# Kernel optimization log

Measured on AMD Instinct MI355X. Metric: run time of the kernel, lower is better.

The kernel has to match this reference:

```python
import jax, jax.numpy as jnp
import numpy as np

N, E, B, D, DEPTH = 20000, 160000, 16, 128, 5
L = 4 * DEPTH  # 20 EGNN layer calls: (ground, ground_to_sub, sub, sub_to_ground) x depth


def _ln(x, g, b):
    mu = jnp.mean(x, -1, keepdims=True)
    var = jnp.mean((x - mu) ** 2, -1, keepdims=True)
    return (x - mu) * jax.lax.rsqrt(var + 1e-5) * g + b


def setup_inputs() -> dict:
    key = jax.random.key(0)
    ks = jax.random.split(key, 24)

    def w(k, shape, fan_in):
        return jax.random.normal(k, shape, jnp.float32) / np.float32(np.sqrt(fan_in))

    return {
        "x": jax.random.normal(ks[0], (N, 1), jnp.float32),
        "pos": jax.random.normal(ks[1], (N, 3), jnp.float32),
        "edge_index": jax.random.randint(ks[2], (2, E), 0, N),
        "node_subnode_index": jax.random.randint(ks[3], (2, E), 0, N),
        "subgraph_edge_index": jax.random.randint(ks[4], (2, E), 0, N),
        "subnode_node_index": jax.random.randint(ks[5], (2, E), 0, N),
        "batch_ids": jnp.sort(jax.random.randint(ks[6], (N,), 0, B)),
        "emb_W": w(ks[7], (1, D), 1), "emb_b": jnp.zeros((D,), jnp.float32),
        # message MLP: Linear(2D+1,D) -> LN -> SiLU -> Linear(D,D) -> LN -> SiLU, stacked over L layers
        "Wm1": w(ks[8], (L, 2 * D + 1, D), 2 * D + 1), "bm1": jnp.zeros((L, D), jnp.float32),
        "gm1": jnp.ones((L, D), jnp.float32), "sm1": jnp.zeros((L, D), jnp.float32),
        "Wm2": w(ks[9], (L, D, D), D), "bm2": jnp.zeros((L, D), jnp.float32),
        "gm2": jnp.ones((L, D), jnp.float32), "sm2": jnp.zeros((L, D), jnp.float32),
        # update MLP: Linear(2D,D) -> LN -> SiLU -> Linear(D,D) -> LN -> SiLU
        "Wu1": w(ks[10], (L, 2 * D, D), 2 * D), "bu1": jnp.zeros((L, D), jnp.float32),
        "gu1": jnp.ones((L, D), jnp.float32), "su1": jnp.zeros((L, D), jnp.float32),
        "Wu2": w(ks[11], (L, D, D), D), "bu2": jnp.zeros((L, D), jnp.float32),
        "gu2": jnp.ones((L, D), jnp.float32), "su2": jnp.zeros((L, D), jnp.float32),
        # prediction head: Linear(D,D) -> ReLU -> Linear(D,1)
        "pred_W1": w(ks[12], (D, D), D), "pred_b1": jnp.zeros((D,), jnp.float32),
        "pred_W2": w(ks[13], (D, 1), D), "pred_b2": jnp.zeros((1,), jnp.float32),
    }


def _egnn(h, pos, ei, i, Wm1, bm1, gm1, sm1, Wm2, bm2, gm2, sm2,
          Wu1, bu1, gu1, su1, Wu2, bu2, gu2, su2):
    src, dst = ei[0], ei[1]          # PyG: messages flow source -> target
    rel = pos[dst] - pos[src]
    dist = jnp.sqrt(jnp.sum(rel * rel, -1, keepdims=True))  # [E,1]
    m = jnp.concatenate([h[dst], h[src], dist], -1)          # [E, 2D+1] = [h_i, h_j, d]
    m = jax.nn.silu(_ln(m @ Wm1[i] + bm1[i], gm1[i], sm1[i]))
    m = jax.nn.silu(_ln(m @ Wm2[i] + bm2[i], gm2[i], sm2[i]))
    agg = jax.ops.segment_sum(m, dst, num_segments=h.shape[0])
    u = jnp.concatenate([h, agg], -1)                        # [N, 2D]
    u = jax.nn.silu(_ln(u @ Wu1[i] + bu1[i], gu1[i], su1[i]))
    u = jax.nn.silu(_ln(u @ Wu2[i] + bu2[i], gu2[i], su2[i]))
    return u


def reference(x, pos, edge_index, node_subnode_index, subgraph_edge_index,
              subnode_node_index, batch_ids, emb_W, emb_b,
              Wm1, bm1, gm1, sm1, Wm2, bm2, gm2, sm2,
              Wu1, bu1, gu1, su1, Wu2, bu2, gu2, su2,
              pred_W1, pred_b1, pred_W2, pred_b2):
    p = (Wm1, bm1, gm1, sm1, Wm2, bm2, gm2, sm2,
         Wu1, bu1, gu1, su1, Wu2, bu2, gu2, su2)
    h = x @ emb_W + emb_b
    edge_sets = (edge_index, node_subnode_index, subgraph_edge_index, subnode_node_index)
    for layer_idx in range(DEPTH):
        h0 = h
        for r, ei in enumerate(edge_sets):
            h = _egnn(h, pos, ei, layer_idx * 4 + r, *p)
        h = h + h0  # residual across the 4 message-passing steps
    out = jax.ops.segment_sum(h, batch_ids, num_segments=B)  # global_add_pool
    return jax.nn.relu(out @ pred_W1 + pred_b1) @ pred_W2 + pred_b2
```

## Files before the change

### kernel.cpp

```cpp
#include <hip/hip_runtime.h>

#define NN 20000
#define NE 160000
#define NL 20

typedef float f32x4 __attribute__((ext_vector_type(4)));
typedef float f32x2 __attribute__((ext_vector_type(2)));
typedef __bf16 bf16x8 __attribute__((ext_vector_type(8)));
typedef __bf16 bf16x4 __attribute__((ext_vector_type(4)));

__device__ __forceinline__ float silu_f(float v) {
  return v * __builtin_amdgcn_rcpf(1.f + __expf(-v));
}

__global__ void pack_weights(const float* __restrict__ W, __bf16* __restrict__ out,
                             const int K, const int lstride, const int total) {
  const int idx = blockIdx.x * 256 + threadIdx.x;
  if (idx >= total) return;
  const int lane = idx & 63;
  const int nt = (idx >> 6) & 7;
  const int ktn = K >> 5;
  const int kt = (idx >> 9) % ktn;
  const int layer = (idx >> 9) / ktn;
  const int col = nt * 16 + (lane & 15);
  const int kb = kt * 32 + (lane >> 4) * 8;
  const float* src = W + (size_t)layer * lstride;
  __bf16* o = out + (size_t)idx * 8;
#pragma unroll
  for (int j = 0; j < 8; ++j) o[j] = (__bf16)src[(kb + j) * 128 + col];
}

__global__ void pack_w1pq(const float* __restrict__ Wm1, __bf16* __restrict__ out) {
  const int idx = blockIdx.x * 256 + threadIdx.x;
  const int lane = idx & 63;
  const int nt = (idx >> 6) & 15;
  const int kt = (idx >> 10) & 3;
  const int layer = idx >> 12;
  const int c = nt * 16 + (lane & 15);
  const int kb = kt * 32 + (lane >> 4) * 8;
  const float* src = Wm1 + (size_t)layer * 257 * 128;
  __bf16* o = out + (size_t)idx * 8;
#pragma unroll
  for (int j = 0; j < 8; ++j) {
    const int k = kb + j;
    o[j] = (__bf16)((c < 128) ? src[k * 128 + c] : src[(128 + k) * 128 + (c - 128)]);
  }
}

__global__ void embed_kernel(const float* __restrict__ x, const float* __restrict__ embW,
                             const float* __restrict__ embB,
                             float* __restrict__ h, float* __restrict__ h0,
                             __bf16* __restrict__ hbf) {
  const int idx = blockIdx.x * 256 + threadIdx.x;
  const int n = idx >> 7, d = idx & 127;
  const float v = x[n] * embW[d] + embB[d];
  h[idx] = v;
  h0[idx] = v;
  hbf[idx] = (__bf16)v;
}

__global__ void hist_kernel(const int* __restrict__ ei, int* __restrict__ deg) {
  const int e = blockIdx.x * 256 + threadIdx.x;
  atomicAdd(&deg[ei[NE + e]], 1);
}

__global__ void scan_kernel(const int* __restrict__ deg, int* __restrict__ rowstart) {
  __shared__ int part[1024];
  const int r = blockIdx.x, t = threadIdx.x;
  const int* d = deg + (size_t)r * NN;
  int* rs = rowstart + (size_t)r * NN;
  int loc[20];
  int cnt = 0;
#pragma unroll
  for (int j = 0; j < 20; ++j) {
    const int i = t * 20 + j;
    const int v = (i < NN) ? d[i] : 0;
    loc[j] = cnt; cnt += v;
  }
  part[t] = cnt;
  __syncthreads();
  for (int off = 1; off < 1024; off <<= 1) {
    const int v = (t >= off) ? part[t - off] : 0;
    __syncthreads();
    part[t] += v;
    __syncthreads();
  }
  const int excl = (t == 0) ? 0 : part[t - 1];
#pragma unroll
  for (int j = 0; j < 20; ++j) {
    const int i = t * 20 + j;
    if (i < NN) rs[i] = excl + loc[j];
  }
}

__global__ void fill_kernel(const int* __restrict__ ei, const int* __restrict__ rowstart,
                            int* __restrict__ cursor, int* __restrict__ eord) {
  const int e = blockIdx.x * 256 + threadIdx.x;
  const int d = ei[NE + e];
  const int p = atomicAdd(&cursor[d], 1);
  eord[rowstart[d] + p] = e;
}

__global__ __launch_bounds__(256) void pq_kernel(
    const __bf16* __restrict__ hbf, const __bf16* __restrict__ pqw,
    __bf16* __restrict__ pq) {
  __shared__ __bf16 T1s[4][2048];
  const int t = threadIdx.x, w = t >> 6, l = t & 63;
  const int lr = l & 15, lg = l >> 4;
  const int wid = blockIdx.x * 4 + w;
  const int n0 = (wid >> 1) * 16;
  const int half = wid & 1;
  char* T1 = (char*)T1s[w];

  const int node = n0 + lr;
  bf16x8 bq[4];
#pragma unroll
  for (int kt = 0; kt < 4; ++kt)
    bq[kt] = *(const bf16x8*)(hbf + (size_t)node * 128 + kt * 32 + lg * 8);

  f32x4 acc[8];
#pragma unroll
  for (int nt = 0; nt < 8; ++nt) acc[nt] = (f32x4)0.f;
#pragma unroll
  for (int kt = 0; kt < 4; ++kt) {
#pragma unroll
    for (int nt = 0; nt < 8; ++nt) {
      const bf16x8 a = *(const bf16x8*)(pqw + ((size_t)((kt * 16 + half * 8 + nt) * 64 + l)) * 8);
      acc[nt] = __builtin_amdgcn_mfma_f32_16x16x32_bf16(a, bq[kt], acc[nt], 0, 0, 0);
    }
  }
#pragma unroll
  for (int nt = 0; nt < 8; ++nt) {
    bf16x4 v;
#pragma unroll
    for (int r = 0; r < 4; ++r) v[r] = (__bf16)acc[nt][r];
    *(bf16x4*)(T1 + ((lr * 256 + nt * 32 + lg * 8) ^ ((lr & 7) << 4))) = v;
  }
  __builtin_amdgcn_s_waitcnt(0);
#pragma unroll
  for (int j = 0; j < 4; ++j) {
    const int row = j * 4 + lg;
    const uint4 v = *(const uint4*)(T1 + ((row * 256 + lr * 16) ^ ((row & 7) << 4)));
    *(uint4*)(pq + (size_t)(n0 + row) * 256 + half * 128 + lr * 8) = v;
  }
}

__global__ __launch_bounds__(1024, 4) void edge_msg_kernel(
    const __bf16* __restrict__ pq, const float* __restrict__ pos,
    const int* __restrict__ ei, __bf16* __restrict__ msg,
    const __bf16* __restrict__ w2p, const float* __restrict__ w1last,
    const float* __restrict__ bm1, const float* __restrict__ gm1, const float* __restrict__ sm1,
    const float* __restrict__ bm2, const float* __restrict__ gm2, const float* __restrict__ sm2) {
  extern __shared__ char lds[];
  {
    const int t = threadIdx.x;
    uint4* d = (uint4*)lds;
    const uint4* s2 = (const uint4*)w2p;
    d[t] = s2[t];
    d[t + 1024] = s2[t + 1024];
  }
  __syncthreads();

  const int t = threadIdx.x, w = t >> 6, l = t & 63;
  const int lr = l & 15, lg = l >> 4;
  char* W2L = lds;
  char* T1  = lds + 32768 + w * 4096;

  const int e0 = blockIdx.x * 256 + w * 16;
  const int es = ei[e0 + lr], ed = ei[NE + e0 + lr];
  const float dx = pos[ed * 3 + 0] - pos[es * 3 + 0];
  const float dy = pos[ed * 3 + 1] - pos[es * 3 + 1];
  const float dz = pos[ed * 3 + 2] - pos[es * 3 + 2];
  const float dist = sqrtf(dx * dx + dy * dy + dz * dz);

  float v[4][8];
#pragma unroll
  for (int kt = 0; kt < 4; ++kt) {
    const int d0 = kt * 32 + lg * 8;
    const bf16x8 pA = *(const bf16x8*)(pq + (size_t)ed * 256 + d0);
    const bf16x8 qA = *(const bf16x8*)(pq + (size_t)es * 256 + 128 + d0);
    const f32x4 wl0 = *(const f32x4*)(w1last + d0), wl1 = *(const f32x4*)(w1last + d0 + 4);
    const f32x4 bb0 = *(const f32x4*)(bm1 + d0),    bb1 = *(const f32x4*)(bm1 + d0 + 4);
#pragma unroll
    for (int j = 0; j < 4; ++j) {
      v[kt][j]     = (float)pA[j]     + (float)qA[j]     + dist * wl0[j] + bb0[j];
      v[kt][j + 4] = (float)pA[j + 4] + (float)qA[j + 4] + dist * wl1[j] + bb1[j];
    }
  }
  float s = 0.f, q = 0.f;
#pragma unroll
  for (int kt = 0; kt < 4; ++kt)
#pragma unroll
    for (int j = 0; j < 8; ++j) { const float x = v[kt][j]; s += x; q += x * x; }
  s += __shfl_xor(s, 16); q += __shfl_xor(q, 16);
  s += __shfl_xor(s, 32); q += __shfl_xor(q, 32);
  const float mu1 = s * 0.0078125f;
  const float rstd1 = rsqrtf(q * 0.0078125f - mu1 * mu1 + 1e-5f);
  bf16x8 bfrag[4];
#pragma unroll
  for (int kt = 0; kt < 4; ++kt) {
    const int d0 = kt * 32 + lg * 8;
    const f32x4 g0 = *(const f32x4*)(gm1 + d0), g1 = *(const f32x4*)(gm1 + d0 + 4);
    const f32x4 s0 = *(const f32x4*)(sm1 + d0), s1 = *(const f32x4*)(sm1 + d0 + 4);
    bf16x8 bf;
#pragma unroll
    for (int j = 0; j < 4; ++j) {
      bf[j]     = (__bf16)silu_f((v[kt][j]     - mu1) * rstd1 * g0[j] + s0[j]);
      bf[j + 4] = (__bf16)silu_f((v[kt][j + 4] - mu1) * rstd1 * g1[j] + s1[j]);
    }
    bfrag[kt] = bf;
  }
  f32x4 acc2[8];
#pragma unroll
  for (int nt = 0; nt < 8; ++nt)
    acc2[nt] = *(const f32x4*)(bm2 + nt * 16 + lg * 4);
#pragma unroll
  for (int kt = 0; kt < 4; ++kt) {
#pragma unroll
    for (int nt = 0; nt < 8; ++nt) {
      const bf16x8 a = *(const bf16x8*)(W2L + ((kt * 8 + nt) * 64 + l) * 16);
      acc2[nt] = __builtin_amdgcn_mfma_f32_16x16x32_bf16(a, bfrag[kt], acc2[nt], 0, 0, 0);
    }
  }
  float s2 = 0.f, q2 = 0.f;
#pragma unroll
  for (int nt = 0; nt < 8; ++nt)
#pragma unroll
    for (int r = 0; r < 4; ++r) { const float x = acc2[nt][r]; s2 += x; q2 += x * x; }
  s2 += __shfl_xor(s2, 16); q2 += __shfl_xor(q2, 16);
  s2 += __shfl_xor(s2, 32); q2 += __shfl_xor(q2, 32);
  const float mu2 = s2 * 0.0078125f;
  const float rstd2 = rsqrtf(q2 * 0.0078125f - mu2 * mu2 + 1e-5f);
#pragma unroll
  for (int nt = 0; nt < 8; ++nt) {
    const f32x4 g2 = *(const f32x4*)(gm2 + nt * 16 + lg * 4);
    const f32x4 b2 = *(const f32x4*)(sm2 + nt * 16 + lg * 4);
    bf16x4 pk;
#pragma unroll
    for (int r = 0; r < 4; ++r)
      pk[r] = (__bf16)silu_f((acc2[nt][r] - mu2) * rstd2 * g2[r] + b2[r]);
    *(bf16x4*)(T1 + ((lr * 256 + nt * 32 + lg * 8) ^ ((lr & 7) << 4))) = pk;
  }
  __builtin_amdgcn_s_waitcnt(0);
  char* mbase = (char*)(msg + (size_t)e0 * 128);
#pragma unroll
  for (int j = 0; j < 4; ++j) {
    const int row = j * 4 + lg;
    const uint4 val = *(const uint4*)(T1 + ((row * 256 + lr * 16) ^ ((row & 7) << 4)));
    *(uint4*)(mbase + j * 1024 + l * 16) = val;
  }
}

__global__ void gather_kernel(const __bf16* __restrict__ msg,
                              const int* __restrict__ rowstart, const int* __restrict__ deg,
                              const int* __restrict__ eord, float* __restrict__ agg) {
  const int t = blockIdx.x * 256 + threadIdx.x;
  const int n = t >> 6, pd = t & 63;
  const int s = rowstart[n], dg = deg[n];
  float a0 = 0.f, a1 = 0.f;
  int i = 0;
  for (; i + 2 <= dg; i += 2) {
    const unsigned v0 = *(const unsigned*)(msg + (size_t)eord[s + i] * 128 + pd * 2);
    const unsigned v1 = *(const unsigned*)(msg + (size_t)eord[s + i + 1] * 128 + pd * 2);
    a0 += __uint_as_float(v0 << 16) + __uint_as_float(v1 << 16);
    a1 += __uint_as_float(v0 & 0xFFFF0000u) + __uint_as_float(v1 & 0xFFFF0000u);
  }
  if (i < dg) {
    const unsigned v0 = *(const unsigned*)(msg + (size_t)eord[s + i] * 128 + pd * 2);
    a0 += __uint_as_float(v0 << 16);
    a1 += __uint_as_float(v0 & 0xFFFF0000u);
  }
  f32x2 o; o[0] = a0; o[1] = a1;
  *(f32x2*)(agg + (size_t)n * 128 + pd * 2) = o;
}

__global__ __launch_bounds__(256) void update_kernel(
    float* __restrict__ h, const float* __restrict__ aggv, __bf16* __restrict__ hbf,
    float* __restrict__ h0, const int mode,
    const __bf16* __restrict__ w1p, const __bf16* __restrict__ w2p,
    const float* __restrict__ bu1, const float* __restrict__ gu1, const float* __restrict__ su1,
    const float* __restrict__ bu2, const float* __restrict__ gu2, const float* __restrict__ su2) {
  __shared__ __bf16 T1s[4][16 * 128];
  const int t = threadIdx.x, w = t >> 6, l = t & 63;
  const int lr = l & 15, lg = l >> 4;
  char* T1 = (char*)T1s[w];
  const int n0 = blockIdx.x * 64 + w * 16;
  const int n = n0 + lr;
  const int valid = (n < NN);
  const int nc = valid ? n : 0;

  bf16x8 ah[4], af[4];
#pragma unroll
  for (int kt = 0; kt < 4; ++kt) {
    ah[kt] = *(const bf16x8*)(hbf + (size_t)nc * 128 + kt * 32 + lg * 8);
    const f32x4* pA = (const f32x4*)(aggv + (size_t)nc * 128 + kt * 32 + lg * 8);
    const f32x4 u0 = pA[0], u1 = pA[1];
#pragma unroll
    for (int j = 0; j < 4; ++j) {
      af[kt][j] = (__bf16)u0[j];
      af[kt][j + 4] = (__bf16)u1[j];
    }
  }
  f32x4 acc[8];
#pragma unroll
  for (int nt = 0; nt < 8; ++nt) {
    const float bb = bu1[nt * 16 + lr];
#pragma unroll
    for (int r = 0; r < 4; ++r) acc[nt][r] = bb;
  }
#pragma unroll
  for (int kt = 0; kt < 8; ++kt) {
    const bf16x8 a = (kt < 4) ? ah[kt] : af[kt - 4];
#pragma unroll
    for (int nt = 0; nt < 8; ++nt) {
      const bf16x8 b = *(const bf16x8*)(w1p + ((size_t)((kt * 8 + nt) * 64 + l)) * 8);
      acc[nt] = __builtin_amdgcn_mfma_f32_16x16x32_bf16(a, b, acc[nt], 0, 0, 0);
    }
  }
  {
    float g1c[8], s1c[8];
#pragma unroll
    for (int nt = 0; nt < 8; ++nt) { g1c[nt] = gu1[nt * 16 + lr]; s1c[nt] = su1[nt * 16 + lr]; }
#pragma unroll
    for (int r = 0; r < 4; ++r) {
      float s = 0.f, q = 0.f;
#pragma unroll
      for (int nt = 0; nt < 8; ++nt) { const float v = acc[nt][r]; s += v; q += v * v; }
#pragma unroll
      for (int m = 1; m < 16; m <<= 1) { s += __shfl_xor(s, m); q += __shfl_xor(q, m); }
      const float mu = s * 0.0078125f;
      const float rstd = rsqrtf(q * 0.0078125f - mu * mu + 1e-5f);
      const int row = lg * 4 + r;
#pragma unroll
      for (int nt = 0; nt < 8; ++nt) {
        float v = (acc[nt][r] - mu) * rstd * g1c[nt] + s1c[nt];
        v = silu_f(v);
        const int col = nt * 16 + lr;
        *(__bf16*)(T1 + ((row * 256 + col * 2) ^ ((row & 7) << 4))) = (__bf16)v;
      }
    }
  }
  __syncthreads();
  f32x4 acc2[8];
#pragma unroll
  for (int nt = 0; nt < 8; ++nt) {
    const float bb = bu2[nt * 16 + lr];
#pragma unroll
    for (int r = 0; r < 4; ++r) acc2[nt][r] = bb;
  }
#pragma unroll
  for (int kt = 0; kt < 4; ++kt) {
    const bf16x8 a = *(const bf16x8*)(T1 + ((lr * 256 + kt * 64 + lg * 16) ^ ((lr & 7) << 4)));
#pragma unroll
    for (int nt = 0; nt < 8; ++nt) {
      const bf16x8 b = *(const bf16x8*)(w2p + ((size_t)((kt * 8 + nt) * 64 + l)) * 8);
      acc2[nt] = __builtin_amdgcn_mfma_f32_16x16x32_bf16(a, b, acc2[nt], 0, 0, 0);
    }
  }
  {
    float g2c[8], s2c[8];
#pragma unroll
    for (int nt = 0; nt < 8; ++nt) { g2c[nt] = gu2[nt * 16 + lr]; s2c[nt] = su2[nt * 16 + lr]; }
#pragma unroll
    for (int r = 0; r < 4; ++r) {
      float s = 0.f, q = 0.f;
#pragma unroll
      for (int nt = 0; nt < 8; ++nt) { const float v = acc2[nt][r]; s += v; q += v * v; }
#pragma unroll
      for (int m = 1; m < 16; m <<= 1) { s += __shfl_xor(s, m); q += __shfl_xor(q, m); }
      const float mu = s * 0.0078125f;
      const float rstd = rsqrtf(q * 0.0078125f - mu * mu + 1e-5f);
      const int row = lg * 4 + r;
      const int nn = n0 + row;
      if (nn < NN) {
#pragma unroll
        for (int nt = 0; nt < 8; ++nt) {
          const int col = nt * 16 + lr;
          float v = (acc2[nt][r] - mu) * rstd * g2c[nt] + s2c[nt];
          v = silu_f(v);
          if (mode) v += h0[(size_t)nn * 128 + col];
          h[(size_t)nn * 128 + col] = v;
          hbf[(size_t)nn * 128 + col] = (__bf16)v;
          if (mode) h0[(size_t)nn * 128 + col] = v;
        }
      }
    }
  }
}

__global__ void pool_kernel(const float* __restrict__ h, const int* __restrict__ bid,
                            float* __restrict__ pooled) {
  const int d = threadIdx.x;
  const int n0 = blockIdx.x * 32;
  const int nend = (n0 + 32 < NN) ? (n0 + 32) : NN;
  float acc = 0.f;
  int cur = bid[n0];
  for (int n = n0; n < nend; ++n) {
    const int b = bid[n];
    if (b != cur) { atomicAdd(&pooled[cur * 128 + d], acc); acc = 0.f; cur = b; }
    acc += h[(size_t)n * 128 + d];
  }
  atomicAdd(&pooled[cur * 128 + d], acc);
}

__global__ void head_kernel(const float* __restrict__ pooled,
                            const float* __restrict__ W1, const float* __restrict__ b1,
                            const float* __restrict__ W2, const float* __restrict__ b2,
                            float* __restrict__ out) {
  __shared__ float buf[2];
  const int b = blockIdx.x, t = threadIdx.x;
  float s = b1[t];
  for (int k = 0; k < 128; ++k) s += pooled[b * 128 + k] * W1[k * 128 + t];
  s = fmaxf(s, 0.f) * W2[t];
#pragma unroll
  for (int m = 32; m >= 1; m >>= 1) s += __shfl_down(s, m);
  if ((t & 63) == 0) buf[t >> 6] = s;
  __syncthreads();
  if (t == 0) out[b] = buf[0] + buf[1] + b2[0];
}

extern "C" void kernel_launch(void* const* d_in, const int* in_sizes, int n_in,
                              void* d_out, int out_size, void* d_ws, size_t ws_size,
                              hipStream_t stream) {
  const float* x   = (const float*)d_in[0];
  const float* pos = (const float*)d_in[1];
  const int* eis[4] = {(const int*)d_in[2], (const int*)d_in[3],
                       (const int*)d_in[4], (const int*)d_in[5]};
  const int* bid = (const int*)d_in[6];
  const float* embW = (const float*)d_in[7];
  const float* embB = (const float*)d_in[8];
  const float* Wm1 = (const float*)d_in[9];
  const float* bm1 = (const float*)d_in[10];
  const float* gm1 = (const float*)d_in[11];
  const float* sm1 = (const float*)d_in[12];
  const float* Wm2 = (const float*)d_in[13];
  const float* bm2 = (const float*)d_in[14];
  const float* gm2 = (const float*)d_in[15];
  const float* sm2 = (const float*)d_in[16];
  const float* Wu1 = (const float*)d_in[17];
  const float* bu1 = (const float*)d_in[18];
  const float* gu1 = (const float*)d_in[19];
  const float* su1 = (const float*)d_in[20];
  const float* Wu2 = (const float*)d_in[21];
  const float* bu2 = (const float*)d_in[22];
  const float* gu2 = (const float*)d_in[23];
  const float* su2 = (const float*)d_in[24];
  const float* pW1 = (const float*)d_in[25];
  const float* pb1 = (const float*)d_in[26];
  const float* pW2 = (const float*)d_in[27];
  const float* pb2 = (const float*)d_in[28];
  float* out = (float*)d_out;

  char* wp = (char*)d_ws;
  float* h = (float*)wp;      wp += (size_t)NN * 128 * 4;
  float* h0 = (float*)wp;     wp += (size_t)NN * 128 * 4;
  float* agg = (float*)wp;    wp += (size_t)NN * 128 * 4;
  float* pooled = (float*)wp; wp += 16 * 128 * 4;
  __bf16* hbf = (__bf16*)wp;  wp += (size_t)NN * 128 * 2;
  __bf16* pq = (__bf16*)wp;   wp += (size_t)NN * 256 * 2;
  __bf16* msg = (__bf16*)wp;  wp += (size_t)NE * 128 * 2;
  __bf16* pqw = (__bf16*)wp;  wp += (size_t)NL * 32768 * 2;
  __bf16* w2p = (__bf16*)wp;  wp += (size_t)NL * 16384 * 2;
  __bf16* wu1p = (__bf16*)wp; wp += (size_t)NL * 32768 * 2;
  __bf16* wu2p = (__bf16*)wp; wp += (size_t)NL * 16384 * 2;
  int* deg = (int*)wp;        wp += (size_t)4 * NN * 4;
  int* cursor = (int*)wp;     wp += (size_t)4 * NN * 4;
  int* rowstart = (int*)wp;   wp += (size_t)4 * NN * 4;
  int* eord = (int*)wp;       wp += (size_t)4 * NE * 4;

  static int lds_attr_set = 0;
  if (!lds_attr_set) {
    hipFuncSetAttribute((const void*)edge_msg_kernel,
                        hipFuncAttributeMaxDynamicSharedMemorySize, 98304);
    lds_attr_set = 1;
  }

  pack_w1pq<<<320, 256, 0, stream>>>(Wm1, pqw);
  pack_weights<<<160, 256, 0, stream>>>(Wm2, w2p, 128, 128 * 128, NL * 4 * 8 * 64);
  pack_weights<<<320, 256, 0, stream>>>(Wu1, wu1p, 256, 256 * 128, NL * 8 * 8 * 64);
  pack_weights<<<160, 256, 0, stream>>>(Wu2, wu2p, 128, 128 * 128, NL * 4 * 8 * 64);

  hipMemsetAsync(deg, 0, (size_t)8 * NN * 4, stream);
  embed_kernel<<<(NN * 128) / 256, 256, 0, stream>>>(x, embW, embB, h, h0, hbf);
  for (int r = 0; r < 4; ++r)
    hist_kernel<<<NE / 256, 256, 0, stream>>>(eis[r], deg + (size_t)r * NN);
  scan_kernel<<<4, 1024, 0, stream>>>(deg, rowstart);
  for (int r = 0; r < 4; ++r)
    fill_kernel<<<NE / 256, 256, 0, stream>>>(eis[r], rowstart + (size_t)r * NN,
                                              cursor + (size_t)r * NN, eord + (size_t)r * NE);

  for (int layer = 0; layer < 5; ++layer) {
    for (int r = 0; r < 4; ++r) {
      const int i = layer * 4 + r;
      pq_kernel<<<625, 256, 0, stream>>>(hbf, pqw + (size_t)i * 32768, pq);
      edge_msg_kernel<<<NE / 256, 1024, 98304, stream>>>(
          pq, pos, eis[r], msg,
          w2p + (size_t)i * 16384,
          Wm1 + (size_t)i * 257 * 128 + 256 * 128,
          bm1 + i * 128, gm1 + i * 128, sm1 + i * 128,
          bm2 + i * 128, gm2 + i * 128, sm2 + i * 128);
      gather_kernel<<<(NN * 64) / 256, 256, 0, stream>>>(
          msg, rowstart + (size_t)r * NN, deg + (size_t)r * NN, eord + (size_t)r * NE, agg);
      update_kernel<<<(NN + 63) / 64, 256, 0, stream>>>(
          h, agg, hbf, h0, (r == 3) ? 1 : 0,
          wu1p + (size_t)i * 32768, wu2p + (size_t)i * 16384,
          bu1 + i * 128, gu1 + i * 128, su1 + i * 128,
          bu2 + i * 128, gu2 + i * 128, su2 + i * 128);
    }
  }

  hipMemsetAsync(pooled, 0, 16 * 128 * 4, stream);
  pool_kernel<<<(NN + 31) / 32, 128, 0, stream>>>(h, bid, pooled);
  head_kernel<<<16, 128, 0, stream>>>(pooled, pW1, pb1, pW2, pb2, out);
}
```

Measured before the change: 1.944 ms.

## Make edge message kernel persistent with register prefetch of next tile

```diff
diff --git a/kernel.cpp b/kernel.cpp
--- a/kernel.cpp
+++ b/kernel.cpp
@@ -136,7 +136,6 @@
     for (int r = 0; r < 4; ++r) v[r] = (__bf16)acc[nt][r];
     *(bf16x4*)(T1 + ((lr * 256 + nt * 32 + lg * 8) ^ ((lr & 7) << 4))) = v;
   }
-  __builtin_amdgcn_s_waitcnt(0);
 #pragma unroll
   for (int j = 0; j < 4; ++j) {
     const int row = j * 4 + lg;
@@ -166,88 +165,120 @@
   char* W2L = lds;
   char* T1  = lds + 32768 + w * 4096;
 
-  const int e0 = blockIdx.x * 256 + w * 16;
-  const int es = ei[e0 + lr], ed = ei[NE + e0 + lr];
-  const float dx = pos[ed * 3 + 0] - pos[es * 3 + 0];
-  const float dy = pos[ed * 3 + 1] - pos[es * 3 + 1];
-  const float dz = pos[ed * 3 + 2] - pos[es * 3 + 2];
-  const float dist = sqrtf(dx * dx + dy * dy + dz * dz);
-
-  float v[4][8];
+  const int NW = gridDim.x * 16;
+  const int NT = NE / 16;
+  int tile = blockIdx.x * 16 + w;
+
+  int es = ei[tile * 16 + lr], ed = ei[NE + tile * 16 + lr];
+  float dist;
+  {
+    const float dx = pos[ed * 3 + 0] - pos[es * 3 + 0];
+    const float dy = pos[ed * 3 + 1] - pos[es * 3 + 1];
+    const float dz = pos[ed * 3 + 2] - pos[es * 3 + 2];
+    dist = sqrtf(dx * dx + dy * dy + dz * dz);
+  }
+  bf16x8 pA[4], qA[4];
 #pragma unroll
   for (int kt = 0; kt < 4; ++kt) {
-    const int d0 = kt * 32 + lg * 8;
-    const bf16x8 pA = *(const bf16x8*)(pq + (size_t)ed * 256 + d0);
-    const bf16x8 qA = *(const bf16x8*)(pq + (size_t)es * 256 + 128 + d0);
-    const f32x4 wl0 = *(const f32x4*)(w1last + d0), wl1 = *(const f32x4*)(w1last + d0 + 4);
-    const f32x4 bb0 = *(const f32x4*)(bm1 + d0),    bb1 = *(const f32x4*)(bm1 + d0 + 4);
+    pA[kt] = *(const bf16x8*)(pq + (size_t)ed * 256 + kt * 32 + lg * 8);
+    qA[kt] = *(const bf16x8*)(pq + (size_t)es * 256 + 128 + kt * 32 + lg * 8);
+  }
+
+  while (true) {
+    const int next = tile + NW;
+    const bool more = (next < NT);
+    float dist_n = 0.f;
+    bf16x8 pA_n[4], qA_n[4];
+    if (more) {
+      const int es_n = ei[next * 16 + lr], ed_n = ei[NE + next * 16 + lr];
+      const float dx = pos[ed_n * 3 + 0] - pos[es_n * 3 + 0];
+      const float dy = pos[ed_n * 3 + 1] - pos[es_n * 3 + 1];
+      const float dz = pos[ed_n * 3 + 2] - pos[es_n * 3 + 2];
+      dist_n = sqrtf(dx * dx + dy * dy + dz * dz);
+#pragma unroll
+      for (int kt = 0; kt < 4; ++kt) {
+        pA_n[kt] = *(const bf16x8*)(pq + (size_t)ed_n * 256 + kt * 32 + lg * 8);
+        qA_n[kt] = *(const bf16x8*)(pq + (size_t)es_n * 256 + 128 + kt * 32 + lg * 8);
+      }
+    }
+    float v[4][8];
+#pragma unroll
+    for (int kt = 0; kt < 4; ++kt) {
+      const int d0 = kt * 32 + lg * 8;
+      const f32x4 wl0 = *(const f32x4*)(w1last + d0), wl1 = *(const f32x4*)(w1last + d0 + 4);
+      const f32x4 bb0 = *(const f32x4*)(bm1 + d0),    bb1 = *(const f32x4*)(bm1 + d0 + 4);
+#pragma unroll
+      for (int j = 0; j < 4; ++j) {
+        v[kt][j]     = (float)pA[kt][j]     + (float)qA[kt][j]     + dist * wl0[j] + bb0[j];
+        v[kt][j + 4] = (float)pA[kt][j + 4] + (float)qA[kt][j + 4] + dist * wl1[j] + bb1[j];
+      }
+    }
+    float s = 0.f, q = 0.f;
+#pragma unroll
+    for (int kt = 0; kt < 4; ++kt)
+#pragma unroll
+      for (int j = 0; j < 8; ++j) { const float x = v[kt][j]; s += x; q += x * x; }
+    s += __shfl_xor(s, 16); q += __shfl_xor(q, 16);
+    s += __shfl_xor(s, 32); q += __shfl_xor(q, 32);
+    const float mu1 = s * 0.0078125f;
+    const float rstd1 = rsqrtf(q * 0.0078125f - mu1 * mu1 + 1e-5f);
+    bf16x8 bfrag[4];
+#pragma unroll
+    for (int kt = 0; kt < 4; ++kt) {
+      const int d0 = kt * 32 + lg * 8;
+      const f32x4 g0 = *(const f32x4*)(gm1 + d0), g1 = *(const f32x4*)(gm1 + d0 + 4);
+      const f32x4 s0 = *(const f32x4*)(sm1 + d0), s1 = *(const f32x4*)(sm1 + d0 + 4);
+      bf16x8 bf;
+#pragma unroll
+      for (int j = 0; j < 4; ++j) {
+        bf[j]     = (__bf16)silu_f((v[kt][j]     - mu1) * rstd1 * g0[j] + s0[j]);
+        bf[j + 4] = (__bf16)silu_f((v[kt][j + 4] - mu1) * rstd1 * g1[j] + s1[j]);
+      }
+      bfrag[kt] = bf;
+    }
+    f32x4 acc2[8];
+#pragma unroll
+    for (int nt = 0; nt < 8; ++nt)
+      acc2[nt] = *(const f32x4*)(bm2 + nt * 16 + lg * 4);
+#pragma unroll
+    for (int kt = 0; kt < 4; ++kt) {
+#pragma unroll
+      for (int nt = 0; nt < 8; ++nt) {
+        const bf16x8 a = *(const bf16x8*)(W2L + ((kt * 8 + nt) * 64 + l) * 16);
+        acc2[nt] = __builtin_amdgcn_mfma_f32_16x16x32_bf16(a, bfrag[kt], acc2[nt], 0, 0, 0);
+      }
+    }
+    float s2 = 0.f, q2 = 0.f;
+#pragma unroll
+    for (int nt = 0; nt < 8; ++nt)
+#pragma unroll
+      for (int r = 0; r < 4; ++r) { const float x = acc2[nt][r]; s2 += x; q2 += x * x; }
+    s2 += __shfl_xor(s2, 16); q2 += __shfl_xor(q2, 16);
+    s2 += __shfl_xor(s2, 32); q2 += __shfl_xor(q2, 32);
+    const float mu2 = s2 * 0.0078125f;
+    const float rstd2 = rsqrtf(q2 * 0.0078125f - mu2 * mu2 + 1e-5f);
+#pragma unroll
+    for (int nt = 0; nt < 8; ++nt) {
+      const f32x4 g2 = *(const f32x4*)(gm2 + nt * 16 + lg * 4);
+      const f32x4 b2 = *(const f32x4*)(sm2 + nt * 16 + lg * 4);
+      bf16x4 pk;
+#pragma unroll
+      for (int r = 0; r < 4; ++r)
+        pk[r] = (__bf16)silu_f((acc2[nt][r] - mu2) * rstd2 * g2[r] + b2[r]);
+      *(bf16x4*)(T1 + ((lr * 256 + nt * 32 + lg * 8) ^ ((lr & 7) << 4))) = pk;
+    }
+    char* mbase = (char*)(msg + (size_t)(tile * 16) * 128);
 #pragma unroll
     for (int j = 0; j < 4; ++j) {
-      v[kt][j]     = (float)pA[j]     + (float)qA[j]     + dist * wl0[j] + bb0[j];
-      v[kt][j + 4] = (float)pA[j + 4] + (float)qA[j + 4] + dist * wl1[j] + bb1[j];
-    }
-  }
-  float s = 0.f, q = 0.f;
-#pragma unroll
-  for (int kt = 0; kt < 4; ++kt)
-#pragma unroll
-    for (int j = 0; j < 8; ++j) { const float x = v[kt][j]; s += x; q += x * x; }
-  s += __shfl_xor(s, 16); q += __shfl_xor(q, 16);
-  s += __shfl_xor(s, 32); q += __shfl_xor(q, 32);
-  const float mu1 = s * 0.0078125f;
-  const float rstd1 = rsqrtf(q * 0.0078125f - mu1 * mu1 + 1e-5f);
-  bf16x8 bfrag[4];
-#pragma unroll
-  for (int kt = 0; kt < 4; ++kt) {
-    const int d0 = kt * 32 + lg * 8;
-    const f32x4 g0 = *(const f32x4*)(gm1 + d0), g1 = *(const f32x4*)(gm1 + d0 + 4);
-    const f32x4 s0 = *(const f32x4*)(sm1 + d0), s1 = *(const f32x4*)(sm1 + d0 + 4);
-    bf16x8 bf;
-#pragma unroll
-    for (int j = 0; j < 4; ++j) {
-      bf[j]     = (__bf16)silu_f((v[kt][j]     - mu1) * rstd1 * g0[j] + s0[j]);
-      bf[j + 4] = (__bf16)silu_f((v[kt][j + 4] - mu1) * rstd1 * g1[j] + s1[j]);
-    }
-    bfrag[kt] = bf;
-  }
-  f32x4 acc2[8];
-#pragma unroll
-  for (int nt = 0; nt < 8; ++nt)
-    acc2[nt] = *(const f32x4*)(bm2 + nt * 16 + lg * 4);
-#pragma unroll
-  for (int kt = 0; kt < 4; ++kt) {
-#pragma unroll
-    for (int nt = 0; nt < 8; ++nt) {
-      const bf16x8 a = *(const bf16x8*)(W2L + ((kt * 8 + nt) * 64 + l) * 16);
-      acc2[nt] = __builtin_amdgcn_mfma_f32_16x16x32_bf16(a, bfrag[kt], acc2[nt], 0, 0, 0);
-    }
-  }
-  float s2 = 0.f, q2 = 0.f;
-#pragma unroll
-  for (int nt = 0; nt < 8; ++nt)
-#pragma unroll
-    for (int r = 0; r < 4; ++r) { const float x = acc2[nt][r]; s2 += x; q2 += x * x; }
-  s2 += __shfl_xor(s2, 16); q2 += __shfl_xor(q2, 16);
-  s2 += __shfl_xor(s2, 32); q2 += __shfl_xor(q2, 32);
-  const float mu2 = s2 * 0.0078125f;
-  const float rstd2 = rsqrtf(q2 * 0.0078125f - mu2 * mu2 + 1e-5f);
-#pragma unroll
-  for (int nt = 0; nt < 8; ++nt) {
-    const f32x4 g2 = *(const f32x4*)(gm2 + nt * 16 + lg * 4);
-    const f32x4 b2 = *(const f32x4*)(sm2 + nt * 16 + lg * 4);
-    bf16x4 pk;
-#pragma unroll
-    for (int r = 0; r < 4; ++r)
-      pk[r] = (__bf16)silu_f((acc2[nt][r] - mu2) * rstd2 * g2[r] + b2[r]);
-    *(bf16x4*)(T1 + ((lr * 256 + nt * 32 + lg * 8) ^ ((lr & 7) << 4))) = pk;
-  }
-  __builtin_amdgcn_s_waitcnt(0);
-  char* mbase = (char*)(msg + (size_t)e0 * 128);
-#pragma unroll
-  for (int j = 0; j < 4; ++j) {
-    const int row = j * 4 + lg;
-    const uint4 val = *(const uint4*)(T1 + ((row * 256 + lr * 16) ^ ((row & 7) << 4)));
-    *(uint4*)(mbase + j * 1024 + l * 16) = val;
+      const int row = j * 4 + lg;
+      const uint4 val = *(const uint4*)(T1 + ((row * 256 + lr * 16) ^ ((row & 7) << 4)));
+      *(uint4*)(mbase + j * 1024 + l * 16) = val;
+    }
+    if (!more) break;
+    tile = next;
+    dist = dist_n;
+#pragma unroll
+    for (int kt = 0; kt < 4; ++kt) { pA[kt] = pA_n[kt]; qA[kt] = qA_n[kt]; }
   }
 }
 
@@ -493,7 +524,7 @@
     for (int r = 0; r < 4; ++r) {
       const int i = layer * 4 + r;
       pq_kernel<<<625, 256, 0, stream>>>(hbf, pqw + (size_t)i * 32768, pq);
-      edge_msg_kernel<<<NE / 256, 1024, 98304, stream>>>(
+      edge_msg_kernel<<<256, 1024, 98304, stream>>>(
           pq, pos, eis[r], msg,
           w2p + (size_t)i * 16384,
           Wm1 + (size_t)i * 257 * 128 + 256 * 128,
```

New measurement: 7.714 ms. 3.97x slower.
